# Kernel optimization log

Hardware: AMD Instinct MI355X
Metric: run time of the kernel (lower is better)

The kernel has to match this reference:

```python
import jax, jax.numpy as jnp
import numpy as np


def setup_inputs() -> dict:
    key = jax.random.key(0)
    k = jax.random.split(key, 5)
    B, N, F = 1024, 256, 6
    H, O = 128, 64
    return {
        "x": jax.random.normal(k[0], (B, N, F), dtype=jnp.float32),
        "W1": jax.random.normal(k[1], (F, H), dtype=jnp.float32) * 0.2,
        "b1": jax.random.normal(k[2], (H,), dtype=jnp.float32) * 0.1,
        "W2": jax.random.normal(k[3], (H, O), dtype=jnp.float32) * 0.1,
        "b2": jax.random.normal(k[4], (O,), dtype=jnp.float32) * 0.1,
    }


def _gcn_norm_adj(x, valid):
    """Dense, vectorized version of the per-batch edge loop + GCN normalization.

    Edge (i,j), i!=j, exists among valid nodes iff cond_i or cond_j, where
    cond = (feat[3] != 0) or (feat[4] != 0). GCNConv adds self-loops on the
    valid subgraph and applies symmetric D^{-1/2} (A+I) D^{-1/2} normalization.
    """
    B, N, _ = x.shape
    cond = (x[..., 3] != 0) | (x[..., 4] != 0)              # [B, N]
    pair = cond[:, :, None] | cond[:, None, :]              # [B, N, N]
    vv = valid[:, :, None] & valid[:, None, :]
    not_diag = ~jnp.eye(N, dtype=bool)[None]
    off = (pair & vv & not_diag).astype(x.dtype)            # off-diagonal edges
    self_loops = jnp.eye(N, dtype=x.dtype)[None] * valid[:, :, None].astype(x.dtype)
    A = off + self_loops                                    # [B, N, N]
    deg = A.sum(-1)                                         # [B, N]
    dinv = jnp.where(deg > 0, jax.lax.rsqrt(jnp.maximum(deg, 1.0)) * (deg > 0), 0.0)
    dinv = jnp.where(deg > 0, deg ** -0.5, 0.0)
    return dinv[:, :, None] * A * dinv[:, None, :]          # [B, N, N]


def reference(x, W1, b1, W2, b2):
    # valid node mask: any nonzero feature
    valid = jnp.abs(x).sum(-1) != 0                         # [B, N]
    An = _gcn_norm_adj(x, valid)

    # GCNConv 1: aggregate(norm_adj, x @ W1) + b1, then ReLU
    h = jax.nn.relu(jnp.einsum("bij,bjh->bih", An, x @ W1) + b1)
    # GCNConv 2
    h = jnp.einsum("bij,bjo->bio", An, h @ W2) + b2         # [B, N, O]

    # global mean pool over valid nodes only (invalid rows excluded)
    vm = valid.astype(h.dtype)
    summed = jnp.einsum("bno,bn->bo", h, vm)
    cnt = vm.sum(-1, keepdims=True)                         # [B, 1]
    return jnp.where(cnt > 0, summed / jnp.maximum(cnt, 1.0), 0.0)
```

## Files before the change

kernel.cpp:

```cpp
#include <hip/hip_runtime.h>
#include <math.h>


#define NB 1024
#define NN 256
#define NF 6
#define NH 128
#define NO 64

template <int CTRL, int ROW_MASK, int BANK_MASK>
__device__ __forceinline__ float dpp_add(float v) {
    int moved = __builtin_amdgcn_update_dpp(0, __float_as_int(v),
                                            CTRL, ROW_MASK, BANK_MASK, true);
    return v + __int_as_float(moved);
}

__device__ __forceinline__ float wave_sum64(float v) {
    v = dpp_add<0x111, 0xf, 0xf>(v);
    v = dpp_add<0x112, 0xf, 0xf>(v);
    v = dpp_add<0x114, 0xf, 0xe>(v);
    v = dpp_add<0x118, 0xf, 0xc>(v);
    v = dpp_add<0x142, 0xa, 0xf>(v);
    v = dpp_add<0x143, 0xc, 0xf>(v);
    return v;
}

__device__ __forceinline__ float bcast63(float v) {
    return __int_as_float(__builtin_amdgcn_readlane(__float_as_int(v), 63));
}

__device__ __forceinline__ float rdlane(float v, int l) {
    return __int_as_float(__builtin_amdgcn_readlane(__float_as_int(v), l));
}

__global__ __launch_bounds__(64) void gnn_kernel(
    const float* __restrict__ x,
    const float* __restrict__ W1,
    const float* __restrict__ b1,
    const float* __restrict__ W2,
    const float* __restrict__ b2,
    float* __restrict__ out)
{
    const int b    = blockIdx.x;
    const int lane = threadIdx.x;

    float w1a[NF], w1b[NF];
    #pragma unroll
    for (int f = 0; f < NF; ++f) {
        w1a[f] = W1[f * NH + lane];
        w1b[f] = W1[f * NH + lane + 64];
    }
    const float b1a = b1[lane];
    const float b1b = b1[lane + 64];
    const float b2r = b2[lane];

    const float4* xp = (const float4*)(x + (size_t)b * NN * NF
                                         + (size_t)lane * 4 * NF);
    float4 q0 = xp[0], q1 = xp[1], q2 = xp[2], q3 = xp[3], q4 = xp[4], q5 = xp[5];
    float xf[4][NF] = {
        { q0.x, q0.y, q0.z, q0.w, q1.x, q1.y },
        { q1.z, q1.w, q2.x, q2.y, q2.z, q2.w },
        { q3.x, q3.y, q3.z, q3.w, q4.x, q4.y },
        { q4.z, q4.w, q5.x, q5.y, q5.z, q5.w },
    };

    bool ncf[4];
    float r[12];
    #pragma unroll
    for (int j = 0; j < 12; ++j) r[j] = 0.f;
    int nv = 0, nc = 0, nnc = 0;

    #pragma unroll
    for (int k = 0; k < 4; ++k) {
        float absum = fabsf(xf[k][0]) + fabsf(xf[k][1]) + fabsf(xf[k][2])
                    + fabsf(xf[k][3]) + fabsf(xf[k][4]) + fabsf(xf[k][5]);
        const bool valid = (absum != 0.f);
        const bool condv = valid && ((xf[k][3] != 0.f) || (xf[k][4] != 0.f));
        const bool isNC  = valid && !condv;
        ncf[k] = isNC;

        nv  += (int)__popcll(__ballot(valid));
        nc  += (int)__popcll(__ballot(condv));
        nnc += (int)__popcll(__ballot(isNC));

        if (condv) {
            #pragma unroll
            for (int f = 0; f < NF; ++f) r[f] += xf[k][f];
        } else if (isNC) {
            #pragma unroll
            for (int f = 0; f < NF; ++f) r[f + 6] += xf[k][f];
        }
    }

    #pragma unroll
    for (int j = 0; j < 12; ++j) r[j] = wave_sum64(r[j]);
    float fs[12];
    #pragma unroll
    for (int j = 0; j < 12; ++j) fs[j] = bcast63(r[j]);

    if (nv == 0) {
        out[(size_t)b * NO + lane] = 0.f;
        return;
    }

    const float a  = 1.f / sqrtf((float)nv);
    const float c  = 1.f / sqrtf((float)(nc + 1));
    const float c2 = c * c;

    float zc0 = 0.f, zn0 = 0.f, zc1 = 0.f, zn1 = 0.f;
    #pragma unroll
    for (int f = 0; f < NF; ++f) {
        zc0 = fmaf(fs[f],     w1a[f], zc0);
        zn0 = fmaf(fs[f + 6], w1a[f], zn0);
        zc1 = fmaf(fs[f],     w1b[f], zc1);
        zn1 = fmaf(fs[f + 6], w1b[f], zn1);
    }
    const float Sc0   = a * zc0,       Sc1   = a * zc1;
    const float Sall0 = Sc0 + c * zn0, Sall1 = Sc1 + c * zn1;

    const float hCa = fmaxf(fmaf(a, Sall0, b1a), 0.f);
    const float hCb = fmaxf(fmaf(a, Sall1, b1b), 0.f);

    float acc0 = 0.f, acc1 = 0.f;
    if (nnc > 0) {
        const float vl0 = fmaf(c, Sc0, b1a);
        const float vl1 = fmaf(c, Sc1, b1b);
        #pragma unroll
        for (int k = 0; k < 4; ++k) {
            unsigned long long m = __ballot(ncf[k]);
            while (m) {
                const int l = (int)__ffsll((long long)m) - 1;
                m &= m - 1;
                float sf[NF];
                #pragma unroll
                for (int f = 0; f < NF; ++f) sf[f] = rdlane(xf[k][f], l);
                float z0 = 0.f, z1 = 0.f;
                #pragma unroll
                for (int f = 0; f < NF; ++f) {
                    z0 = fmaf(sf[f], w1a[f], z0);
                    z1 = fmaf(sf[f], w1b[f], z1);
                }
                acc0 += fmaxf(fmaf(c2, z0, vl0), 0.f);
                acc1 += fmaxf(fmaf(c2, z1, vl1), 0.f);
            }
        }
    }

    const float alpha = a * (float)nc * ((float)nc * a + (float)(nv - nc) * c);
    const float beta  = c * ((float)nc * a + c);
    const float inv_nv = 1.f / (float)nv;
    const float ga = (alpha * hCa + beta * acc0) * inv_nv;
    const float gb = (alpha * hCb + beta * acc1) * inv_nv;

    float y = 0.f;
    #pragma unroll
    for (int hh = 0; hh < 64; ++hh) {
        y = fmaf(rdlane(ga, hh), W2[hh * NO + lane],        y);
        y = fmaf(rdlane(gb, hh), W2[(hh + 64) * NO + lane], y);
    }

    out[(size_t)b * NO + lane] = y + b2r;
}

extern "C" void kernel_launch(void* const* d_in, const int* in_sizes, int n_in,
                              void* d_out, int out_size, void* d_ws, size_t ws_size,
                              hipStream_t stream) {
    const float* x  = (const float*)d_in[0];
    const float* W1 = (const float*)d_in[1];
    const float* b1 = (const float*)d_in[2];
    const float* W2 = (const float*)d_in[3];
    const float* b2 = (const float*)d_in[4];
    float* out = (float*)d_out;

    gnn_kernel<<<NB, 64, 0, stream>>>(x, W1, b1, W2, b2, out);
}
```

Baseline: 10.22 us.

## Split each graph across two waves with LDS-compacted non-cond nodes

Each block now runs two wavefronts, each owning half the nodes and half of the hidden units. Partial sums and counts go through shared memory. Non-cond nodes are compacted into an LDS list so every lane loops over them directly instead of using serialized readlane broadcasts. W2 is preloaded into registers, and the two waves' output partials are combined through LDS. This doubles per-block parallelism and shortens the serial dependency chains, at the cost of two barriers, more LDS, and higher register pressure.

Measured after the change: 9.372 us. 1.09x faster.

```diff
diff --git a/kernel.cpp b/kernel.cpp
--- a/kernel.cpp
+++ b/kernel.cpp
@@ -25,15 +25,11 @@
     return v;
 }
 
-__device__ __forceinline__ float bcast63(float v) {
-    return __int_as_float(__builtin_amdgcn_readlane(__float_as_int(v), 63));
-}
-
 __device__ __forceinline__ float rdlane(float v, int l) {
     return __int_as_float(__builtin_amdgcn_readlane(__float_as_int(v), l));
 }
 
-__global__ __launch_bounds__(64) void gnn_kernel(
+__global__ __launch_bounds__(128) void gnn_kernel(
     const float* __restrict__ x,
     const float* __restrict__ W1,
     const float* __restrict__ b1,
@@ -42,36 +38,42 @@
     float* __restrict__ out)
 {
     const int b    = blockIdx.x;
-    const int lane = threadIdx.x;
-
-    float w1a[NF], w1b[NF];
-    #pragma unroll
-    for (int f = 0; f < NF; ++f) {
-        w1a[f] = W1[f * NH + lane];
-        w1b[f] = W1[f * NH + lane + 64];
-    }
-    const float b1a = b1[lane];
-    const float b1b = b1[lane + 64];
-    const float b2r = b2[lane];
+    const int t    = threadIdx.x;
+    const int wid  = t >> 6;
+    const int lane = t & 63;
+    const int h    = (wid << 6) + lane;
+
+    __shared__ float  psum[2][16];
+    __shared__ float4 xc4[NN][2];
+    __shared__ float  ypart[NO];
 
     const float4* xp = (const float4*)(x + (size_t)b * NN * NF
-                                         + (size_t)lane * 4 * NF);
-    float4 q0 = xp[0], q1 = xp[1], q2 = xp[2], q3 = xp[3], q4 = xp[4], q5 = xp[5];
-    float xf[4][NF] = {
+                                         + (size_t)((wid << 7) + lane * 2) * NF);
+    float4 q0 = xp[0], q1 = xp[1], q2 = xp[2];
+    float xf[2][NF] = {
         { q0.x, q0.y, q0.z, q0.w, q1.x, q1.y },
         { q1.z, q1.w, q2.x, q2.y, q2.z, q2.w },
-        { q3.x, q3.y, q3.z, q3.w, q4.x, q4.y },
-        { q4.z, q4.w, q5.x, q5.y, q5.z, q5.w },
     };
 
-    bool ncf[4];
+    float w1r[NF];
+    #pragma unroll
+    for (int f = 0; f < NF; ++f) w1r[f] = W1[f * NH + h];
+    const float b1r = b1[h];
+    const float b2r = b2[lane];
+    float w2r[64];
+    #pragma unroll
+    for (int hh = 0; hh < 64; ++hh)
+        w2r[hh] = W2[(size_t)(((wid << 6) + hh) * NO) + lane];
+
+    bool ncf[2];
+    unsigned long long mN0, mN1;
     float r[12];
     #pragma unroll
     for (int j = 0; j < 12; ++j) r[j] = 0.f;
-    int nv = 0, nc = 0, nnc = 0;
-
-    #pragma unroll
-    for (int k = 0; k < 4; ++k) {
+    int nvw = 0, ncw = 0;
+
+    #pragma unroll
+    for (int k = 0; k < 2; ++k) {
         float absum = fabsf(xf[k][0]) + fabsf(xf[k][1]) + fabsf(xf[k][2])
                     + fabsf(xf[k][3]) + fabsf(xf[k][4]) + fabsf(xf[k][5]);
         const bool valid = (absum != 0.f);
@@ -79,9 +81,9 @@
         const bool isNC  = valid && !condv;
         ncf[k] = isNC;
 
-        nv  += (int)__popcll(__ballot(valid));
-        nc  += (int)__popcll(__ballot(condv));
-        nnc += (int)__popcll(__ballot(isNC));
+        nvw += (int)__popcll(__ballot(valid));
+        ncw += (int)__popcll(__ballot(condv));
+        if (k == 0) mN0 = __ballot(isNC); else mN1 = __ballot(isNC);
 
         if (condv) {
             #pragma unroll
@@ -91,15 +93,44 @@
             for (int f = 0; f < NF; ++f) r[f + 6] += xf[k][f];
         }
     }
+    const int c0   = (int)__popcll(mN0);
+    const int nncw = c0 + (int)__popcll(mN1);
 
     #pragma unroll
     for (int j = 0; j < 12; ++j) r[j] = wave_sum64(r[j]);
+    if (lane == 63) {
+        #pragma unroll
+        for (int j = 0; j < 12; ++j) psum[wid][j] = r[j];
+        psum[wid][12] = (float)nvw;
+        psum[wid][13] = (float)ncw;
+        psum[wid][14] = (float)nncw;
+    }
+
+    const unsigned long long ltm = (1ull << lane) - 1ull;
+    if (ncf[0]) {
+        const int rank = (int)__popcll(mN0 & ltm);
+        const int idx  = wid ? (NN - 1 - rank) : rank;
+        xc4[idx][0] = make_float4(xf[0][0], xf[0][1], xf[0][2], xf[0][3]);
+        xc4[idx][1] = make_float4(xf[0][4], xf[0][5], 0.f, 0.f);
+    }
+    if (ncf[1]) {
+        const int rank = c0 + (int)__popcll(mN1 & ltm);
+        const int idx  = wid ? (NN - 1 - rank) : rank;
+        xc4[idx][0] = make_float4(xf[1][0], xf[1][1], xf[1][2], xf[1][3]);
+        xc4[idx][1] = make_float4(xf[1][4], xf[1][5], 0.f, 0.f);
+    }
+    __syncthreads();
+
     float fs[12];
     #pragma unroll
-    for (int j = 0; j < 12; ++j) fs[j] = bcast63(r[j]);
+    for (int j = 0; j < 12; ++j) fs[j] = psum[0][j] + psum[1][j];
+    const int nv   = (int)(psum[0][12] + psum[1][12]);
+    const int nc   = (int)(psum[0][13] + psum[1][13]);
+    const int nnc0 = (int)psum[0][14];
+    const int nnc1 = (int)psum[1][14];
 
     if (nv == 0) {
-        out[(size_t)b * NO + lane] = 0.f;
+        if (wid == 0) out[(size_t)b * NO + lane] = 0.f;
         return;
     }
 
@@ -107,59 +138,59 @@
     const float c  = 1.f / sqrtf((float)(nc + 1));
     const float c2 = c * c;
 
-    float zc0 = 0.f, zn0 = 0.f, zc1 = 0.f, zn1 = 0.f;
+    float zc = 0.f, zn = 0.f;
     #pragma unroll
     for (int f = 0; f < NF; ++f) {
-        zc0 = fmaf(fs[f],     w1a[f], zc0);
-        zn0 = fmaf(fs[f + 6], w1a[f], zn0);
-        zc1 = fmaf(fs[f],     w1b[f], zc1);
-        zn1 = fmaf(fs[f + 6], w1b[f], zn1);
-    }
-    const float Sc0   = a * zc0,       Sc1   = a * zc1;
-    const float Sall0 = Sc0 + c * zn0, Sall1 = Sc1 + c * zn1;
-
-    const float hCa = fmaxf(fmaf(a, Sall0, b1a), 0.f);
-    const float hCb = fmaxf(fmaf(a, Sall1, b1b), 0.f);
-
-    float acc0 = 0.f, acc1 = 0.f;
-    if (nnc > 0) {
-        const float vl0 = fmaf(c, Sc0, b1a);
-        const float vl1 = fmaf(c, Sc1, b1b);
-        #pragma unroll
-        for (int k = 0; k < 4; ++k) {
-            unsigned long long m = __ballot(ncf[k]);
-            while (m) {
-                const int l = (int)__ffsll((long long)m) - 1;
-                m &= m - 1;
-                float sf[NF];
-                #pragma unroll
-                for (int f = 0; f < NF; ++f) sf[f] = rdlane(xf[k][f], l);
-                float z0 = 0.f, z1 = 0.f;
-                #pragma unroll
-                for (int f = 0; f < NF; ++f) {
-                    z0 = fmaf(sf[f], w1a[f], z0);
-                    z1 = fmaf(sf[f], w1b[f], z1);
-                }
-                acc0 += fmaxf(fmaf(c2, z0, vl0), 0.f);
-                acc1 += fmaxf(fmaf(c2, z1, vl1), 0.f);
-            }
+        zc = fmaf(fs[f],     w1r[f], zc);
+        zn = fmaf(fs[f + 6], w1r[f], zn);
+    }
+    const float Sc   = a * zc;
+    const float Sall = Sc + c * zn;
+    const float hC   = fmaxf(fmaf(a, Sall, b1r), 0.f);
+
+    float acc = 0.f;
+    if (nnc0 + nnc1 > 0) {
+        const float vloc = fmaf(c, Sc, b1r);
+        for (int k = 0; k < nnc0; ++k) {
+            const float4 u0 = xc4[k][0];
+            const float4 u1 = xc4[k][1];
+            float z = u0.x * w1r[0];
+            z = fmaf(u0.y, w1r[1], z);
+            z = fmaf(u0.z, w1r[2], z);
+            z = fmaf(u0.w, w1r[3], z);
+            z = fmaf(u1.x, w1r[4], z);
+            z = fmaf(u1.y, w1r[5], z);
+            acc += fmaxf(fmaf(c2, z, vloc), 0.f);
         }
-    }
-
-    const float alpha = a * (float)nc * ((float)nc * a + (float)(nv - nc) * c);
-    const float beta  = c * ((float)nc * a + c);
+        for (int k = NN - nnc1; k < NN; ++k) {
+            const float4 u0 = xc4[k][0];
+            const float4 u1 = xc4[k][1];
+            float z = u0.x * w1r[0];
+            z = fmaf(u0.y, w1r[1], z);
+            z = fmaf(u0.z, w1r[2], z);
+            z = fmaf(u0.w, w1r[3], z);
+            z = fmaf(u1.x, w1r[4], z);
+            z = fmaf(u1.y, w1r[5], z);
+            acc += fmaxf(fmaf(c2, z, vloc), 0.f);
+        }
+    }
+
+    const float alpha  = a * (float)nc * ((float)nc * a + (float)(nv - nc) * c);
+    const float beta   = c * ((float)nc * a + c);
     const float inv_nv = 1.f / (float)nv;
-    const float ga = (alpha * hCa + beta * acc0) * inv_nv;
-    const float gb = (alpha * hCb + beta * acc1) * inv_nv;
-
-    float y = 0.f;
-    #pragma unroll
-    for (int hh = 0; hh < 64; ++hh) {
-        y = fmaf(rdlane(ga, hh), W2[hh * NO + lane],        y);
-        y = fmaf(rdlane(gb, hh), W2[(hh + 64) * NO + lane], y);
-    }
-
-    out[(size_t)b * NO + lane] = y + b2r;
+    const float g = (alpha * hC + beta * acc) * inv_nv;
+
+    float y0 = 0.f, y1 = 0.f;
+    #pragma unroll
+    for (int hh = 0; hh < 64; hh += 2) {
+        y0 = fmaf(rdlane(g, hh),     w2r[hh],     y0);
+        y1 = fmaf(rdlane(g, hh + 1), w2r[hh + 1], y1);
+    }
+    const float y = y0 + y1;
+
+    if (wid == 1) ypart[lane] = y;
+    __syncthreads();
+    if (wid == 0) out[(size_t)b * NO + lane] = y + ypart[lane] + b2r;
 }
 
 extern "C" void kernel_launch(void* const* d_in, const int* in_sizes, int n_in,
@@ -172,5 +203,5 @@
     const float* b2 = (const float*)d_in[4];
     float* out = (float*)d_out;
 
-    gnn_kernel<<<NB, 64, 0, stream>>>(x, W1, b1, W2, b2, out);
-}
+    gnn_kernel<<<NB, 128, 0, stream>>>(x, W1, b1, W2, b2, out);
+}
```
